# Optimization experiments

Hardware: AMD Instinct MI355X
Metric: run time of the kernel (lower is better)

## Reference

```python
import jax, jax.numpy as jnp
import numpy as np

THRESHOLD = 0.01
NT, NS, C = 8192, 8192, 512


def setup_inputs() -> dict:
    key = jax.random.key(0)
    k1, k2 = jax.random.split(key)
    # rows are class probabilities (module takes log of them for NLL)
    td_pre = jax.nn.softmax(jax.random.normal(k1, (NT, C), dtype=jnp.float32), axis=1)
    sd_pre = jax.nn.softmax(jax.random.normal(k2, (NS, C), dtype=jnp.float32), axis=1)
    return {"td_pre": td_pre, "sd_pre": sd_pre}


def reference(td_pre, sd_pre):
    conf_t = jnp.max(td_pre, axis=1)
    lab_t = jnp.argmax(td_pre, axis=1)
    conf_s = jnp.max(sd_pre, axis=1)
    lab_s = jnp.argmax(sd_pre, axis=1)
    mask_t = conf_t > THRESHOLD  # [NT] bool
    mask_s = conf_s > THRESHOLD  # [NS] bool

    # score[i] = sum_j sim[i, j] over j with matching pseudo-label (source rows only kept if mask_s)
    sim = td_pre @ sd_pre.T  # [NT, NS]
    eq = (lab_t[:, None] == lab_s[None, :]) & mask_s[None, :]
    score = jnp.sum(jnp.where(eq, sim, 0.0), axis=1)  # [NT]

    # softmax over the confident target rows only (== torch softmax over compacted vector)
    neg_inf = jnp.float32(-1e30)
    weights = jax.nn.softmax(jnp.where(mask_t, score, neg_inf), axis=0)  # [NT], ~0 at unmasked

    # nll_loss(log(td_pre), lab_t, reduction='none') per row
    loss = -jnp.log(jnp.take_along_axis(td_pre, lab_t[:, None], axis=1)[:, 0])  # [NT]

    cnt = jnp.maximum(jnp.sum(mask_t.astype(jnp.float32)), 1.0)
    weighted_loss = jnp.sum(jnp.where(mask_t, loss * weights, 0.0)) / cnt
    return weighted_loss, mask_t, lab_t, weights
```

## Files before the change

kernel.cpp:

```cpp
#include <hip/hip_runtime.h>
#include <math.h>

#define NT 8192
#define NS 8192
#define C 512
#define THRESH 0.01f

__global__ __launch_bounds__(256) void stc_rowmax_t(
    const float* __restrict__ td, float* __restrict__ out_mask,
    float* __restrict__ out_lab, float* __restrict__ loss, int* __restrict__ labi)
{
    int wave = threadIdx.x >> 6;
    int lane = threadIdx.x & 63;
    int row = blockIdx.x * 4 + wave;
    if (row >= NT) return;
    const float* p = td + (size_t)row * C;
    float best = -1.0f; int bi = 0;
#pragma unroll
    for (int h = 0; h < 2; ++h) {
        int col = h * 256 + lane * 4;
        float4 v = *reinterpret_cast<const float4*>(p + col);
        if (v.x > best) { best = v.x; bi = col; }
        if (v.y > best) { best = v.y; bi = col + 1; }
        if (v.z > best) { best = v.z; bi = col + 2; }
        if (v.w > best) { best = v.w; bi = col + 3; }
    }
#pragma unroll
    for (int off = 32; off; off >>= 1) {
        float ov = __shfl_down(best, off);
        int   oi = __shfl_down(bi, off);
        if (ov > best || (ov == best && oi < bi)) { best = ov; bi = oi; }
    }
    if (lane == 0) {
        out_mask[row] = (best > THRESH) ? 1.0f : 0.0f;
        out_lab[row] = (float)bi;
        loss[row] = -logf(best);
        labi[row] = bi;
    }
}

__global__ __launch_bounds__(256) void stc_rowmax_s(
    const float* __restrict__ sd, int* __restrict__ labm)
{
    int wave = threadIdx.x >> 6;
    int lane = threadIdx.x & 63;
    int row = blockIdx.x * 4 + wave;
    if (row >= NS) return;
    const float* p = sd + (size_t)row * C;
    float best = -1.0f; int bi = 0;
#pragma unroll
    for (int h = 0; h < 2; ++h) {
        int col = h * 256 + lane * 4;
        float4 v = *reinterpret_cast<const float4*>(p + col);
        if (v.x > best) { best = v.x; bi = col; }
        if (v.y > best) { best = v.y; bi = col + 1; }
        if (v.z > best) { best = v.z; bi = col + 2; }
        if (v.w > best) { best = v.w; bi = col + 3; }
    }
#pragma unroll
    for (int off = 32; off; off >>= 1) {
        float ov = __shfl_down(best, off);
        int   oi = __shfl_down(bi, off);
        if (ov > best || (ov == best && oi < bi)) { best = ov; bi = oi; }
    }
    if (lane == 0) {
        labm[row] = (best > THRESH) ? bi : -1;
    }
}

__global__ __launch_bounds__(64) void stc_build_g(
    const float* __restrict__ sd, const int* __restrict__ labm,
    float* __restrict__ gpart, int rows_per_chunk)
{
    const int c = blockIdx.x;
    const int chunk = blockIdx.y;
    const int lane = threadIdx.x;
    const int base0 = chunk * rows_per_chunk;
    float a0 = 0, a1 = 0, a2 = 0, a3 = 0, b0 = 0, b1 = 0, b2 = 0, b3 = 0;
    for (int base = base0; base < base0 + rows_per_chunk; base += 64) {
        int l = labm[base + lane];
        unsigned long long mb = __ballot(l == c);
        while (mb) {
            int b = __ffsll(mb) - 1;
            mb &= mb - 1;
            const float* sp = sd + (size_t)(base + b) * C;
            float4 v0 = *reinterpret_cast<const float4*>(sp + lane * 4);
            float4 v1 = *reinterpret_cast<const float4*>(sp + 256 + lane * 4);
            a0 += v0.x; a1 += v0.y; a2 += v0.z; a3 += v0.w;
            b0 += v1.x; b1 += v1.y; b2 += v1.z; b3 += v1.w;
        }
    }
    float* gp = gpart + ((size_t)chunk * C + c) * C;
    *reinterpret_cast<float4*>(gp + lane * 4)       = make_float4(a0, a1, a2, a3);
    *reinterpret_cast<float4*>(gp + 256 + lane * 4) = make_float4(b0, b1, b2, b3);
}

__global__ __launch_bounds__(256) void stc_reduce_g(
    const float4* __restrict__ gpart, float4* __restrict__ g, int chunks)
{
    int i = blockIdx.x * 256 + threadIdx.x;
    float4 s = gpart[i];
    for (int k = 1; k < chunks; ++k) {
        float4 v = gpart[(size_t)k * (C * C / 4) + i];
        s.x += v.x; s.y += v.y; s.z += v.z; s.w += v.w;
    }
    g[i] = s;
}

__global__ __launch_bounds__(256) void stc_score(
    const float* __restrict__ td, const float* __restrict__ G,
    const int* __restrict__ labi, float* __restrict__ score)
{
    int wave = threadIdx.x >> 6;
    int lane = threadIdx.x & 63;
    int row = blockIdx.x * 4 + wave;
    if (row >= NT) return;
    const float* a = td + (size_t)row * C;
    const float* g = G + (size_t)labi[row] * C;
    float acc = 0.0f;
#pragma unroll
    for (int h = 0; h < 2; ++h) {
        int col = h * 256 + lane * 4;
        float4 x = *reinterpret_cast<const float4*>(a + col);
        float4 y = *reinterpret_cast<const float4*>(g + col);
        acc += x.x * y.x + x.y * y.y + x.z * y.z + x.w * y.w;
    }
#pragma unroll
    for (int off = 32; off; off >>= 1) acc += __shfl_down(acc, off);
    if (lane == 0) score[row] = acc;
}

__global__ __launch_bounds__(1024) void stc_stats(
    const float* __restrict__ score, const float* __restrict__ mask_f,
    const float* __restrict__ loss, float* __restrict__ scal,
    float* __restrict__ out0)
{
    __shared__ float red[1024];
    int t = threadIdx.x;
    float vmax = -1e30f;
    for (int i = t; i < NT; i += 1024) {
        float v = (mask_f[i] != 0.0f) ? score[i] : -1e30f;
        vmax = fmaxf(vmax, v);
    }
    red[t] = vmax; __syncthreads();
    for (int s = 512; s; s >>= 1) {
        if (t < s) red[t] = fmaxf(red[t], red[t + s]);
        __syncthreads();
    }
    float m = red[0]; __syncthreads();

    float se = 0.0f, sle = 0.0f, cnt = 0.0f;
    for (int i = t; i < NT; i += 1024) {
        bool msk = mask_f[i] != 0.0f;
        float v = msk ? score[i] : -1e30f;
        float e = expf(v - m);
        se += e;
        if (msk) { sle += loss[i] * e; cnt += 1.0f; }
    }
    red[t] = se; __syncthreads();
    for (int s = 512; s; s >>= 1) { if (t < s) red[t] += red[t + s]; __syncthreads(); }
    float se_tot = red[0]; __syncthreads();
    red[t] = sle; __syncthreads();
    for (int s = 512; s; s >>= 1) { if (t < s) red[t] += red[t + s]; __syncthreads(); }
    float sle_tot = red[0]; __syncthreads();
    red[t] = cnt; __syncthreads();
    for (int s = 512; s; s >>= 1) { if (t < s) red[t] += red[t + s]; __syncthreads(); }
    float cnt_tot = red[0];

    if (t == 0) {
        scal[0] = m;
        scal[1] = se_tot;
        float c = fmaxf(cnt_tot, 1.0f);
        out0[0] = (sle_tot / se_tot) / c;
    }
}

__global__ __launch_bounds__(256) void stc_weights(
    const float* __restrict__ score, const float* __restrict__ mask_f,
    const float* __restrict__ scal, float* __restrict__ out_w)
{
    int i = blockIdx.x * 256 + threadIdx.x;
    if (i >= NT) return;
    float m = scal[0];
    float se = scal[1];
    float v = (mask_f[i] != 0.0f) ? score[i] : -1e30f;
    out_w[i] = expf(v - m) / se;
}

extern "C" void kernel_launch(void* const* d_in, const int* in_sizes, int n_in,
                              void* d_out, int out_size, void* d_ws, size_t ws_size,
                              hipStream_t stream) {
    const float* td = (const float*)d_in[0];
    const float* sd = (const float*)d_in[1];
    float* out = (float*)d_out;
    float* out_loss = out;
    float* out_mask = out + 1;
    float* out_lab  = out + 1 + NT;
    float* out_w    = out + 1 + 2 * NT;

    char* ws = (char*)d_ws;
    float* loss  = (float*)(ws + 0);
    float* score = (float*)(ws + 32768);
    int*   labm  = (int*)  (ws + 65536);
    int*   labi  = (int*)  (ws + 98304);
    float* scal  = (float*)(ws + 131072);
    float* G     = (float*)(ws + 132096);
    float* Gpart = (float*)(ws + 132096 + (size_t)C * C * 4);

    int chunks = 4;
    size_t need4 = 132096 + (size_t)C * C * 4 * (1 + 4);
    if (ws_size < need4) { chunks = 1; Gpart = G; }
    int rows_per_chunk = NS / chunks;

    stc_rowmax_t<<<NT / 4, 256, 0, stream>>>(td, out_mask, out_lab, loss, labi);
    stc_rowmax_s<<<NS / 4, 256, 0, stream>>>(sd, labm);
    stc_build_g<<<dim3(C, chunks), 64, 0, stream>>>(sd, labm, Gpart, rows_per_chunk);
    if (chunks > 1) {
        stc_reduce_g<<<(C * C / 4) / 256, 256, 0, stream>>>((const float4*)Gpart, (float4*)G, chunks);
    }
    stc_score<<<NT / 4, 256, 0, stream>>>(td, G, labi, score);
    stc_stats<<<1, 1024, 0, stream>>>(score, out_mask, loss, scal, out_loss);
    stc_weights<<<NT / 256, 256, 0, stream>>>(score, out_mask, scal, out_w);
}
```

Measured before the change: 50.27 us.

## Fuse rowmax kernels, fold chunk reduction into score, merge weights into stats

The two row-argmax kernels are merged into one launch covering both matrices. The separate G reduction kernel is removed, and the score kernel instead sums the dot products over each partial chunk of G directly. The weights kernel is folded into the single-block stats kernel. This cuts the launch count from seven to four and skips writing and re-reading the reduced G, at the cost of more gather reads per score row and serial weight writes in one block.

```diff
diff --git a/kernel.cpp b/kernel.cpp
--- a/kernel.cpp
+++ b/kernel.cpp
@@ -6,15 +6,18 @@
 #define C 512
 #define THRESH 0.01f
 
-__global__ __launch_bounds__(256) void stc_rowmax_t(
-    const float* __restrict__ td, float* __restrict__ out_mask,
-    float* __restrict__ out_lab, float* __restrict__ loss, int* __restrict__ labi)
+__global__ __launch_bounds__(256) void stc_rowmax(
+    const float* __restrict__ td, const float* __restrict__ sd,
+    float* __restrict__ out_mask, float* __restrict__ out_lab,
+    float* __restrict__ loss, int* __restrict__ labi, int* __restrict__ labm)
 {
     int wave = threadIdx.x >> 6;
     int lane = threadIdx.x & 63;
-    int row = blockIdx.x * 4 + wave;
-    if (row >= NT) return;
-    const float* p = td + (size_t)row * C;
+    int gw = blockIdx.x * 4 + wave;
+    bool is_t = gw < NT;
+    int row = is_t ? gw : gw - NT;
+    const float* p = (is_t ? td : sd) + (size_t)row * C;
+
     float best = -1.0f; int bi = 0;
 #pragma unroll
     for (int h = 0; h < 2; ++h) {
@@ -32,39 +35,14 @@
         if (ov > best || (ov == best && oi < bi)) { best = ov; bi = oi; }
     }
     if (lane == 0) {
-        out_mask[row] = (best > THRESH) ? 1.0f : 0.0f;
-        out_lab[row] = (float)bi;
-        loss[row] = -logf(best);
-        labi[row] = bi;
-    }
-}
-
-__global__ __launch_bounds__(256) void stc_rowmax_s(
-    const float* __restrict__ sd, int* __restrict__ labm)
-{
-    int wave = threadIdx.x >> 6;
-    int lane = threadIdx.x & 63;
-    int row = blockIdx.x * 4 + wave;
-    if (row >= NS) return;
-    const float* p = sd + (size_t)row * C;
-    float best = -1.0f; int bi = 0;
-#pragma unroll
-    for (int h = 0; h < 2; ++h) {
-        int col = h * 256 + lane * 4;
-        float4 v = *reinterpret_cast<const float4*>(p + col);
-        if (v.x > best) { best = v.x; bi = col; }
-        if (v.y > best) { best = v.y; bi = col + 1; }
-        if (v.z > best) { best = v.z; bi = col + 2; }
-        if (v.w > best) { best = v.w; bi = col + 3; }
-    }
-#pragma unroll
-    for (int off = 32; off; off >>= 1) {
-        float ov = __shfl_down(best, off);
-        int   oi = __shfl_down(bi, off);
-        if (ov > best || (ov == best && oi < bi)) { best = ov; bi = oi; }
-    }
-    if (lane == 0) {
-        labm[row] = (best > THRESH) ? bi : -1;
+        if (is_t) {
+            out_mask[row] = (best > THRESH) ? 1.0f : 0.0f;
+            out_lab[row] = (float)bi;
+            loss[row] = -logf(best);
+            labi[row] = bi;
+        } else {
+            labm[row] = (best > THRESH) ? bi : -1;
+        }
     }
 }
 
@@ -95,45 +73,37 @@
     *reinterpret_cast<float4*>(gp + 256 + lane * 4) = make_float4(b0, b1, b2, b3);
 }
 
-__global__ __launch_bounds__(256) void stc_reduce_g(
-    const float4* __restrict__ gpart, float4* __restrict__ g, int chunks)
-{
-    int i = blockIdx.x * 256 + threadIdx.x;
-    float4 s = gpart[i];
-    for (int k = 1; k < chunks; ++k) {
-        float4 v = gpart[(size_t)k * (C * C / 4) + i];
-        s.x += v.x; s.y += v.y; s.z += v.z; s.w += v.w;
-    }
-    g[i] = s;
-}
-
 __global__ __launch_bounds__(256) void stc_score(
-    const float* __restrict__ td, const float* __restrict__ G,
-    const int* __restrict__ labi, float* __restrict__ score)
+    const float* __restrict__ td, const float* __restrict__ gpart,
+    const int* __restrict__ labi, float* __restrict__ score, int chunks)
 {
     int wave = threadIdx.x >> 6;
     int lane = threadIdx.x & 63;
     int row = blockIdx.x * 4 + wave;
     if (row >= NT) return;
     const float* a = td + (size_t)row * C;
-    const float* g = G + (size_t)labi[row] * C;
+    int lab = labi[row];
+
+    float4 x0 = *reinterpret_cast<const float4*>(a + lane * 4);
+    float4 x1 = *reinterpret_cast<const float4*>(a + 256 + lane * 4);
+
     float acc = 0.0f;
-#pragma unroll
-    for (int h = 0; h < 2; ++h) {
-        int col = h * 256 + lane * 4;
-        float4 x = *reinterpret_cast<const float4*>(a + col);
-        float4 y = *reinterpret_cast<const float4*>(g + col);
-        acc += x.x * y.x + x.y * y.y + x.z * y.z + x.w * y.w;
+    for (int k = 0; k < chunks; ++k) {
+        const float* g = gpart + ((size_t)k * C + lab) * C;
+        float4 y0 = *reinterpret_cast<const float4*>(g + lane * 4);
+        float4 y1 = *reinterpret_cast<const float4*>(g + 256 + lane * 4);
+        acc += x0.x * y0.x + x0.y * y0.y + x0.z * y0.z + x0.w * y0.w;
+        acc += x1.x * y1.x + x1.y * y1.y + x1.z * y1.z + x1.w * y1.w;
     }
 #pragma unroll
     for (int off = 32; off; off >>= 1) acc += __shfl_down(acc, off);
     if (lane == 0) score[row] = acc;
 }
 
-__global__ __launch_bounds__(1024) void stc_stats(
+__global__ __launch_bounds__(1024) void stc_stats_weights(
     const float* __restrict__ score, const float* __restrict__ mask_f,
-    const float* __restrict__ loss, float* __restrict__ scal,
-    float* __restrict__ out0)
+    const float* __restrict__ loss, float* __restrict__ out0,
+    float* __restrict__ out_w)
 {
     __shared__ float red[1024];
     int t = threadIdx.x;
@@ -167,24 +137,13 @@
     for (int s = 512; s; s >>= 1) { if (t < s) red[t] += red[t + s]; __syncthreads(); }
     float cnt_tot = red[0];
 
+    for (int i = t; i < NT; i += 1024) {
+        float v = (mask_f[i] != 0.0f) ? score[i] : -1e30f;
+        out_w[i] = expf(v - m) / se_tot;
+    }
     if (t == 0) {
-        scal[0] = m;
-        scal[1] = se_tot;
-        float c = fmaxf(cnt_tot, 1.0f);
-        out0[0] = (sle_tot / se_tot) / c;
+        out0[0] = (sle_tot / se_tot) / fmaxf(cnt_tot, 1.0f);
     }
-}
-
-__global__ __launch_bounds__(256) void stc_weights(
-    const float* __restrict__ score, const float* __restrict__ mask_f,
-    const float* __restrict__ scal, float* __restrict__ out_w)
-{
-    int i = blockIdx.x * 256 + threadIdx.x;
-    if (i >= NT) return;
-    float m = scal[0];
-    float se = scal[1];
-    float v = (mask_f[i] != 0.0f) ? score[i] : -1e30f;
-    out_w[i] = expf(v - m) / se;
 }
 
 extern "C" void kernel_launch(void* const* d_in, const int* in_sizes, int n_in,
@@ -203,22 +162,16 @@
     float* score = (float*)(ws + 32768);
     int*   labm  = (int*)  (ws + 65536);
     int*   labi  = (int*)  (ws + 98304);
-    float* scal  = (float*)(ws + 131072);
-    float* G     = (float*)(ws + 132096);
-    float* Gpart = (float*)(ws + 132096 + (size_t)C * C * 4);
+    float* Gpart = (float*)(ws + 131072);
 
     int chunks = 4;
-    size_t need4 = 132096 + (size_t)C * C * 4 * (1 + 4);
-    if (ws_size < need4) { chunks = 1; Gpart = G; }
+    if (ws_size < 131072 + (size_t)4 * C * C * 4) {
+        chunks = (ws_size >= 131072 + (size_t)2 * C * C * 4) ? 2 : 1;
+    }
     int rows_per_chunk = NS / chunks;
 
-    stc_rowmax_t<<<NT / 4, 256, 0, stream>>>(td, out_mask, out_lab, loss, labi);
-    stc_rowmax_s<<<NS / 4, 256, 0, stream>>>(sd, labm);
+    stc_rowmax<<<(NT + NS) / 4, 256, 0, stream>>>(td, sd, out_mask, out_lab, loss, labi, labm);
     stc_build_g<<<dim3(C, chunks), 64, 0, stream>>>(sd, labm, Gpart, rows_per_chunk);
-    if (chunks > 1) {
-        stc_reduce_g<<<(C * C / 4) / 256, 256, 0, stream>>>((const float4*)Gpart, (float4*)G, chunks);
-    }
-    stc_score<<<NT / 4, 256, 0, stream>>>(td, G, labi, score);
-    stc_stats<<<1, 1024, 0, stream>>>(score, out_mask, loss, scal, out_loss);
-    stc_weights<<<NT / 256, 256, 0, stream>>>(score, out_mask, scal, out_w);
+    stc_score<<<NT / 4, 256, 0, stream>>>(td, Gpart, labi, score, chunks);
+    stc_stats_weights<<<1, 1024, 0, stream>>>(score, out_mask, loss, out_loss, out_w);
 }
```

Result: no change. 50.18 us (-0.2%).
